# Performance work log

Hardware: AMD Instinct MI355X
Metric: run time of the kernel (lower is better)

The kernel has to match this reference:

```python
import jax, jax.numpy as jnp
import numpy as np

N_NODES = 500_000
N_ELEM = 2_000_000
W_AXIAL = 1.0
W_BENDING = 1.0


def _local_axes(x_local):
    # ref = [0,1,0] unless nearly parallel to x, then [0,0,1]
    parallel = jnp.abs(x_local[:, 1]) > 0.99
    ref = jnp.where(parallel[:, None],
                    jnp.array([0.0, 0.0, 1.0], x_local.dtype),
                    jnp.array([0.0, 1.0, 0.0], x_local.dtype))
    z = jnp.cross(x_local, ref)
    z = z / jnp.maximum(jnp.linalg.norm(z, axis=-1, keepdims=True), 1e-8)
    y = jnp.cross(z, x_local)
    y = y / jnp.maximum(jnp.linalg.norm(y, axis=-1, keepdims=True), 1e-8)
    return y, z


def setup_inputs() -> dict:
    key = jax.random.key(0)
    ks = jax.random.split(key, 10)
    pred = jax.random.normal(ks[0], (N_NODES, 6), jnp.float32) * 0.01
    connectivity = jax.random.randint(ks[1], (N_ELEM, 2), 0, N_NODES, dtype=jnp.int32)
    d = jax.random.normal(ks[2], (N_ELEM, 3), jnp.float32)
    elem_directions = d / jnp.linalg.norm(d, axis=-1, keepdims=True)
    elem_lengths = jax.random.uniform(ks[3], (N_ELEM,), jnp.float32, 0.5, 5.0)
    prop_E = jax.random.uniform(ks[4], (N_ELEM,), jnp.float32, 1e5, 2e6)
    prop_A = jax.random.uniform(ks[5], (N_ELEM,), jnp.float32, 0.01, 0.1)
    prop_I22 = jax.random.uniform(ks[6], (N_ELEM,), jnp.float32, 1e-5, 1e-3)
    line_load = jax.random.normal(ks[7], (N_NODES, 3), jnp.float32)
    bc_disp = jax.random.uniform(ks[8], (N_NODES, 1), jnp.float32)
    bc_rot = jax.random.uniform(ks[9], (N_NODES, 1), jnp.float32)
    return dict(pred=pred, connectivity=connectivity, elem_directions=elem_directions,
                elem_lengths=elem_lengths, prop_E=prop_E, prop_A=prop_A,
                prop_I22=prop_I22, line_load=line_load, bc_disp=bc_disp, bc_rot=bc_rot)


def reference(pred, connectivity, elem_directions, elem_lengths,
              prop_E, prop_A, prop_I22, line_load, bc_disp, bc_rot):
    n_nodes = pred.shape[0]
    u = pred[:, :3]
    theta = pred[:, 3:6]
    i_nodes = connectivity[:, 0]
    j_nodes = connectivity[:, 1]
    x_local = elem_directions
    y_local, z_local = _local_axes(x_local)
    L = elem_lengths

    du = u[j_nodes] - u[i_nodes]            # (E,3)
    th_i = theta[i_nodes]
    th_j = theta[j_nodes]

    # axial
    axial_disp = jnp.sum(du * x_local, axis=-1)
    N_axial = prop_E * prop_A / L * axial_disp
    F_axial_vec = N_axial[:, None] * x_local

    EI = prop_E * prop_I22
    L2 = L * L
    L3 = L2 * L

    # bending: transverse z (rotations about y)
    dw_z = jnp.sum(du * z_local, axis=-1)
    theta_yi = jnp.sum(th_i * y_local, axis=-1)
    theta_yj = jnp.sum(th_j * y_local, axis=-1)
    V_z = 12.0 * EI / L3 * dw_z + 6.0 * EI / L2 * (theta_yi + theta_yj)
    F_shear_vec = V_z[:, None] * z_local
    M_yi = 6.0 * EI / L2 * dw_z + EI / L * (2.0 * theta_yi + theta_yj)
    M_yj = 6.0 * EI / L2 * dw_z + EI / L * (theta_yi + 2.0 * theta_yj)
    M_vec_i = M_yi[:, None] * y_local
    M_vec_j = M_yj[:, None] * y_local

    # bending: transverse y (rotations about z)
    dw_y = jnp.sum(du * y_local, axis=-1)
    theta_zi = jnp.sum(th_i * z_local, axis=-1)
    theta_zj = jnp.sum(th_j * z_local, axis=-1)
    V_y = 12.0 * EI / L3 * dw_y + 6.0 * EI / L2 * (theta_zi + theta_zj)
    F_shear_y_vec = V_y[:, None] * y_local
    M_zi = 6.0 * EI / L2 * dw_y + EI / L * (2.0 * theta_zi + theta_zj)
    M_zj = 6.0 * EI / L2 * dw_y + EI / L * (theta_zi + 2.0 * theta_zj)
    M_vec_zi = M_zi[:, None] * z_local
    M_vec_zj = M_zj[:, None] * z_local

    # scatter to nodes (combined contributions, same sum as six scatter_adds)
    F_contrib = F_axial_vec + F_shear_vec + F_shear_y_vec
    F_total = jnp.zeros((n_nodes, 3), pred.dtype)
    F_total = F_total.at[i_nodes].add(F_contrib).at[j_nodes].add(-F_contrib)
    F_residual = F_total + line_load

    M_total = jnp.zeros((n_nodes, 3), pred.dtype)
    M_total = M_total.at[i_nodes].add(M_vec_i + M_vec_zi).at[j_nodes].add(M_vec_j + M_vec_zj)

    # characteristic scales
    F_char = jnp.maximum(jnp.mean(prop_E * prop_A), 1.0)
    M_char = jnp.maximum(jnp.mean(prop_E * prop_I22 / L), 1.0)

    # masked means over free nodes (== boolean-indexed .mean() in torch)
    free_disp = (bc_disp[:, 0] < 0.5).astype(pred.dtype)   # (N,)
    free_rot = (bc_rot[:, 0] < 0.5).astype(pred.dtype)
    sq_f = (F_residual / F_char) ** 2
    sq_m = (M_total / M_char) ** 2
    loss_force = jnp.sum(sq_f * free_disp[:, None]) / jnp.maximum(jnp.sum(free_disp) * 3.0, 1.0)
    loss_moment = jnp.sum(sq_m * free_rot[:, None]) / jnp.maximum(jnp.sum(free_rot) * 3.0, 1.0)
    return W_AXIAL * loss_force + W_BENDING * loss_moment
```

## Files before the change

### kernel.cpp

```cpp
#include <hip/hip_runtime.h>
#include <hip/hip_bf16.h>

#define N_NODES 500000
#define N_ELEM  2000000

#define CSH   11
#define NPBIN (1 << CSH)
#define NBIN  ((N_NODES + NPBIN - 1) >> CSH)
#define SBLK  256
#define CBLK  512

#define P16_OFF 32768ull
#define ENT_OFF (P16_OFF + 16ull * N_NODES)
#define WS_NEED (ENT_OFF + 16ull * 2 * N_ELEM)

__device__ __forceinline__ float wave_reduce(float v) {
    #pragma unroll
    for (int o = 32; o > 0; o >>= 1) v += __shfl_down(v, o, 64);
    return v;
}

template<int NW>
__device__ __forceinline__ void block_reduce_add(float v, double* dst, float* sm) {
    int lane = threadIdx.x & 63;
    int wave = threadIdx.x >> 6;
    v = wave_reduce(v);
    if (lane == 0) sm[wave] = v;
    __syncthreads();
    if (threadIdx.x == 0) {
        float s = 0.f;
        #pragma unroll
        for (int w = 0; w < NW; ++w) s += sm[w];
        atomicAdd(dst, (double)s);
    }
    __syncthreads();
}

__device__ __forceinline__ unsigned int pack2(float a, float b) {
    unsigned int ua = (__float_as_uint(a) + 0x8000u) >> 16;
    unsigned int ub = (__float_as_uint(b) + 0x8000u) & 0xFFFF0000u;
    return ua | ub;
}
__device__ __forceinline__ float unlo(unsigned int u) {
    return __uint_as_float(u << 16);
}
__device__ __forceinline__ float unhi(unsigned int u) {
    return __uint_as_float(u & 0xFFFF0000u);
}

__device__ __forceinline__ void beam_core(
    float x0, float x1, float x2,
    float u0i, float u1i, float u2i, float t0i, float t1i, float t2i,
    float u0j, float u1j, float u2j, float t0j, float t1j, float t2j,
    float L, float E, float A, float I,
    float& F0, float& F1, float& F2,
    float& Mi0, float& Mi1, float& Mi2,
    float& Mj0, float& Mj1, float& Mj2)
{
    bool par = fabsf(x1) > 0.99f;
    float r1 = par ? 0.f : 1.f;
    float r2 = par ? 1.f : 0.f;
    float z0 = x1 * r2 - x2 * r1;
    float z1 = -x0 * r2;
    float z2 = x0 * r1;
    float zn = fmaxf(sqrtf(z0 * z0 + z1 * z1 + z2 * z2), 1e-8f);
    float izn = 1.f / zn;
    z0 *= izn; z1 *= izn; z2 *= izn;
    float y0 = z1 * x2 - z2 * x1;
    float y1 = z2 * x0 - z0 * x2;
    float y2 = z0 * x1 - z1 * x0;
    float yn = fmaxf(sqrtf(y0 * y0 + y1 * y1 + y2 * y2), 1e-8f);
    float iyn = 1.f / yn;
    y0 *= iyn; y1 *= iyn; y2 *= iyn;

    float du0 = u0j - u0i;
    float du1 = u1j - u1i;
    float du2 = u2j - u2i;

    float EA = E * A;
    float EI = E * I;
    float invL = 1.f / L;
    float invL2 = invL * invL;
    float invL3 = invL2 * invL;

    float axial = du0 * x0 + du1 * x1 + du2 * x2;
    float Naxial = EA * invL * axial;

    float k12 = 12.f * EI * invL3;
    float k6  = 6.f * EI * invL2;
    float kL  = EI * invL;

    float dwz = du0 * z0 + du1 * z1 + du2 * z2;
    float tyi = t0i * y0 + t1i * y1 + t2i * y2;
    float tyj = t0j * y0 + t1j * y1 + t2j * y2;
    float Vz  = k12 * dwz + k6 * (tyi + tyj);
    float Myi = k6 * dwz + kL * (2.f * tyi + tyj);
    float Myj = k6 * dwz + kL * (tyi + 2.f * tyj);

    float dwy = du0 * y0 + du1 * y1 + du2 * y2;
    float tzi = t0i * z0 + t1i * z1 + t2i * z2;
    float tzj = t0j * z0 + t1j * z1 + t2j * z2;
    float Vy  = k12 * dwy + k6 * (tzi + tzj);
    float Mzi = k6 * dwy + kL * (2.f * tzi + tzj);
    float Mzj = k6 * dwy + kL * (tzi + 2.f * tzj);

    F0 = Naxial * x0 + Vz * z0 + Vy * y0;
    F1 = Naxial * x1 + Vz * z1 + Vy * y1;
    F2 = Naxial * x2 + Vz * z2 + Vy * y2;

    Mi0 = Myi * y0 + Mzi * z0;
    Mi1 = Myi * y1 + Mzi * z1;
    Mi2 = Myi * y2 + Mzi * z2;
    Mj0 = Myj * y0 + Mzj * z0;
    Mj1 = Myj * y1 + Mzj * z1;
    Mj2 = Myj * y2 + Mzj * z2;
}

__device__ __forceinline__ void beam_full(
    float x0, float x1, float x2,
    const float* __restrict__ pi, const float* __restrict__ pj,
    float L, float E, float A, float I,
    float& F0, float& F1, float& F2,
    float& Mi0, float& Mi1, float& Mi2,
    float& Mj0, float& Mj1, float& Mj2)
{
    float2 a0 = *(const float2*)(pi + 0);
    float2 a1 = *(const float2*)(pi + 2);
    float2 a2 = *(const float2*)(pi + 4);
    float2 b0 = *(const float2*)(pj + 0);
    float2 b1 = *(const float2*)(pj + 2);
    float2 b2 = *(const float2*)(pj + 4);
    beam_core(x0, x1, x2,
              a0.x, a0.y, a1.x, a1.y, a2.x, a2.y,
              b0.x, b0.y, b1.x, b1.y, b2.x, b2.y,
              L, E, A, I,
              F0, F1, F2, Mi0, Mi1, Mi2, Mj0, Mj1, Mj2);
}


__global__ __launch_bounds__(256) void prep_kernel(
    const float* __restrict__ pred, uint4* __restrict__ pred16)
{
    int n = blockIdx.x * 256 + threadIdx.x;
    if (n >= N_NODES) return;
    const float2* p2 = (const float2*)(pred + 6l * n);
    float2 a0 = p2[0], a1 = p2[1], a2 = p2[2];
    uint4 r;
    r.x = pack2(a0.x, a0.y);
    r.y = pack2(a1.x, a1.y);
    r.z = pack2(a2.x, a2.y);
    r.w = 0u;
    pred16[n] = r;
}


__global__ __launch_bounds__(256) void count_kernel(
    const int* __restrict__ conn, int* __restrict__ cnt)
{
    __shared__ int bins[NBIN];
    for (int i = threadIdx.x; i < NBIN; i += 256) bins[i] = 0;
    __syncthreads();

    int per = (N_ELEM + CBLK - 1) / CBLK;
    int e0 = blockIdx.x * per;
    int e1 = min(e0 + per, N_ELEM);
    const int2* c2 = (const int2*)conn;

    for (int e = e0 + threadIdx.x; e < e1; e += 256) {
        int2 c = c2[e];
        atomicAdd(&bins[c.x >> CSH], 1);
        atomicAdd(&bins[c.y >> CSH], 1);
    }
    __syncthreads();
    for (int i = threadIdx.x; i < NBIN; i += 256) {
        int c = bins[i];
        if (c) atomicAdd(&cnt[i], c);
    }
}

__global__ __launch_bounds__(256) void scan_kernel(
    const int* __restrict__ cnt,
    int* __restrict__ cur, int* __restrict__ off)
{
    __shared__ int s[256];
    int tid = threadIdx.x;
    int v = (tid < NBIN) ? cnt[tid] : 0;
    s[tid] = v;
    __syncthreads();
    for (int o = 1; o < 256; o <<= 1) {
        int t = (tid >= o) ? s[tid - o] : 0;
        __syncthreads();
        s[tid] += t;
        __syncthreads();
    }
    int excl = s[tid] - v;
    if (tid < NBIN) { off[tid] = excl; cur[tid] = excl; }
    if (tid == 255) off[NBIN] = s[255];
}


__global__ __launch_bounds__(1024) void emit_kernel(
    const uint4* __restrict__ pred16,
    const int* __restrict__ conn,
    const float* __restrict__ dirs,
    const float* __restrict__ L_, const float* __restrict__ E_,
    const float* __restrict__ A_, const float* __restrict__ I_,
    int* __restrict__ cur, uint4* __restrict__ ents,
    double* __restrict__ accum)
{
    __shared__ int bins[NBIN];
    __shared__ float sm[16];
    for (int i = threadIdx.x; i < NBIN; i += 1024) bins[i] = 0;
    __syncthreads();

    int per = (N_ELEM + SBLK - 1) / SBLK;
    int e0 = blockIdx.x * per;
    int e1 = min(e0 + per, N_ELEM);
    const int2* c2 = (const int2*)conn;

    for (int e = e0 + threadIdx.x; e < e1; e += 1024) {
        int2 c = c2[e];
        atomicAdd(&bins[c.x >> CSH], 1);
        atomicAdd(&bins[c.y >> CSH], 1);
    }
    __syncthreads();
    for (int i = threadIdx.x; i < NBIN; i += 1024) {
        int c = bins[i];
        bins[i] = c ? atomicAdd(&cur[i], c) : 0;
    }
    __syncthreads();

    float ea = 0.f, eil = 0.f;
    for (int e = e0 + threadIdx.x; e < e1; e += 1024) {
        int2 c = c2[e];
        uint4 pi = pred16[c.x];
        uint4 pj = pred16[c.y];
        float x0 = dirs[3 * e + 0], x1 = dirs[3 * e + 1], x2 = dirs[3 * e + 2];
        float L = L_[e], E = E_[e], A = A_[e], I = I_[e];
        ea  += E * A;
        eil += E * I / L;
        float F0, F1, F2, Mi0, Mi1, Mi2, Mj0, Mj1, Mj2;
        beam_core(x0, x1, x2,
                  unlo(pi.x), unhi(pi.x), unlo(pi.y), unhi(pi.y), unlo(pi.z), unhi(pi.z),
                  unlo(pj.x), unhi(pj.x), unlo(pj.y), unhi(pj.y), unlo(pj.z), unhi(pj.z),
                  L, E, A, I,
                  F0, F1, F2, Mi0, Mi1, Mi2, Mj0, Mj1, Mj2);

        int pi_ = atomicAdd(&bins[c.x >> CSH], 1);
        uint4 ei;
        ei.x = pack2(F0, F1);
        ei.y = pack2(F2, Mi0);
        ei.z = pack2(Mi1, Mi2);
        ei.w = (unsigned int)(c.x & (NPBIN - 1));
        ents[pi_] = ei;

        int pj_ = atomicAdd(&bins[c.y >> CSH], 1);
        uint4 ej;
        ej.x = pack2(-F0, -F1);
        ej.y = pack2(-F2, Mj0);
        ej.z = pack2(Mj1, Mj2);
        ej.w = (unsigned int)(c.y & (NPBIN - 1));
        ents[pj_] = ej;
    }
    block_reduce_add<16>(ea,  &accum[0], sm);
    block_reduce_add<16>(eil, &accum[1], sm);
}


__global__ __launch_bounds__(1024) void binacc_kernel(
    const uint4* __restrict__ ents,
    const int* __restrict__ off,
    const float* __restrict__ line_load,
    const float* __restrict__ bc_disp,
    const float* __restrict__ bc_rot,
    double* __restrict__ accum)
{
    __shared__ unsigned int acc3[NPBIN * 3];
    __shared__ float sm[16];
    int b = blockIdx.x;
    for (int i = threadIdx.x; i < NPBIN * 3; i += 1024) acc3[i] = 0u;
    __syncthreads();

    int s0 = off[b], s1 = off[b + 1];
    int nbase = b << CSH;
    unsigned int lds_base = (unsigned int)(unsigned long long)(&acc3[0]);

    int k = s0 + threadIdx.x;
    for (; k + 1024 < s1; k += 2048) {
        uint4 ea_ = ents[k];
        uint4 eb_ = ents[k + 1024];
        unsigned int aa = lds_base + ea_.w * 12u;
        unsigned int ab = lds_base + eb_.w * 12u;
        asm volatile(
            "ds_pk_add_bf16 %0, %2\n\t"
            "ds_pk_add_bf16 %0, %3 offset:4\n\t"
            "ds_pk_add_bf16 %0, %4 offset:8\n\t"
            "ds_pk_add_bf16 %1, %5\n\t"
            "ds_pk_add_bf16 %1, %6 offset:4\n\t"
            "ds_pk_add_bf16 %1, %7 offset:8"
            :: "v"(aa), "v"(ab),
               "v"(ea_.x), "v"(ea_.y), "v"(ea_.z),
               "v"(eb_.x), "v"(eb_.y), "v"(eb_.z)
            : "memory");
    }
    if (k < s1) {
        uint4 e = ents[k];
        unsigned int a = lds_base + e.w * 12u;
        asm volatile(
            "ds_pk_add_bf16 %0, %1\n\t"
            "ds_pk_add_bf16 %0, %2 offset:4\n\t"
            "ds_pk_add_bf16 %0, %3 offset:8"
            :: "v"(a), "v"(e.x), "v"(e.y), "v"(e.z)
            : "memory");
    }
    asm volatile("s_waitcnt lgkmcnt(0)" ::: "memory");
    __syncthreads();

    float sqF = 0.f, sqM = 0.f, fd = 0.f, fr = 0.f;
    for (int nl = threadIdx.x; nl < NPBIN; nl += 1024) {
        int n = nbase + nl;
        if (n < N_NODES) {
            float fdv = (bc_disp[n] < 0.5f) ? 1.f : 0.f;
            float frv = (bc_rot[n]  < 0.5f) ? 1.f : 0.f;
            unsigned int w0 = acc3[nl * 3 + 0];
            unsigned int w1 = acc3[nl * 3 + 1];
            unsigned int w2 = acc3[nl * 3 + 2];
            float Fr0 = unlo(w0) + line_load[3l * n + 0];
            float Fr1 = unhi(w0) + line_load[3l * n + 1];
            float Fr2 = unlo(w1) + line_load[3l * n + 2];
            float M0 = unhi(w1);
            float M1 = unlo(w2);
            float M2 = unhi(w2);
            sqF += fdv * (Fr0 * Fr0 + Fr1 * Fr1 + Fr2 * Fr2);
            sqM += frv * (M0 * M0 + M1 * M1 + M2 * M2);
            fd += fdv;
            fr += frv;
        }
    }
    block_reduce_add<16>(sqF, &accum[2], sm);
    block_reduce_add<16>(sqM, &accum[3], sm);
    block_reduce_add<16>(fd,  &accum[4], sm);
    block_reduce_add<16>(fr,  &accum[5], sm);
}

__global__ void final_kernel(const double* __restrict__ accum,
                             float* __restrict__ out)
{
    double F_char = fmax(accum[0] / (double)N_ELEM, 1.0);
    double M_char = fmax(accum[1] / (double)N_ELEM, 1.0);
    double lf = accum[2] / (F_char * F_char) / fmax(accum[4] * 3.0, 1.0);
    double lm = accum[3] / (M_char * M_char) / fmax(accum[5] * 3.0, 1.0);
    out[0] = (float)(lf + lm);
}


__global__ __launch_bounds__(256) void elem_kernel_fb(
    const float* __restrict__ pred,
    const int*   __restrict__ conn,
    const float* __restrict__ dirs,
    const float* __restrict__ L_, const float* __restrict__ E_,
    const float* __restrict__ A_, const float* __restrict__ I_,
    float* __restrict__ F_total, float* __restrict__ M_total,
    double* __restrict__ accum)
{
    __shared__ float sm[4];
    int e = blockIdx.x * blockDim.x + threadIdx.x;
    float ea = 0.f, eil = 0.f;
    if (e < N_ELEM) {
        int ni = conn[2 * e], nj = conn[2 * e + 1];
        float x0 = dirs[3 * e + 0], x1 = dirs[3 * e + 1], x2 = dirs[3 * e + 2];
        float L = L_[e], E = E_[e], A = A_[e], I = I_[e];
        float F0, F1, F2, Mi0, Mi1, Mi2, Mj0, Mj1, Mj2;
        beam_full(x0, x1, x2, pred + 6l * ni, pred + 6l * nj, L, E, A, I,
                  F0, F1, F2, Mi0, Mi1, Mi2, Mj0, Mj1, Mj2);
        atomicAdd(&F_total[3l * ni + 0],  F0);
        atomicAdd(&F_total[3l * ni + 1],  F1);
        atomicAdd(&F_total[3l * ni + 2],  F2);
        atomicAdd(&F_total[3l * nj + 0], -F0);
        atomicAdd(&F_total[3l * nj + 1], -F1);
        atomicAdd(&F_total[3l * nj + 2], -F2);
        atomicAdd(&M_total[3l * ni + 0], Mi0);
        atomicAdd(&M_total[3l * ni + 1], Mi1);
        atomicAdd(&M_total[3l * ni + 2], Mi2);
        atomicAdd(&M_total[3l * nj + 0], Mj0);
        atomicAdd(&M_total[3l * nj + 1], Mj1);
        atomicAdd(&M_total[3l * nj + 2], Mj2);
        ea  = E * A;
        eil = E * I / L;
    }
    block_reduce_add<4>(ea,  &accum[0], sm);
    block_reduce_add<4>(eil, &accum[1], sm);
}

__global__ __launch_bounds__(256) void node_kernel_fb(
    const float* __restrict__ F_total, const float* __restrict__ M_total,
    const float* __restrict__ line_load,
    const float* __restrict__ bc_disp, const float* __restrict__ bc_rot,
    double* __restrict__ accum)
{
    __shared__ float sm[4];
    int n = blockIdx.x * blockDim.x + threadIdx.x;
    float sqF = 0.f, sqM = 0.f, fd = 0.f, fr = 0.f;
    if (n < N_NODES) {
        fd = (bc_disp[n] < 0.5f) ? 1.f : 0.f;
        fr = (bc_rot[n]  < 0.5f) ? 1.f : 0.f;
        float Fr0 = F_total[3l * n + 0] + line_load[3l * n + 0];
        float Fr1 = F_total[3l * n + 1] + line_load[3l * n + 1];
        float Fr2 = F_total[3l * n + 2] + line_load[3l * n + 2];
        float M0 = M_total[3l * n + 0];
        float M1 = M_total[3l * n + 1];
        float M2 = M_total[3l * n + 2];
        sqF = fd * (Fr0 * Fr0 + Fr1 * Fr1 + Fr2 * Fr2);
        sqM = fr * (M0 * M0 + M1 * M1 + M2 * M2);
    }
    block_reduce_add<4>(sqF, &accum[2], sm);
    block_reduce_add<4>(sqM, &accum[3], sm);
    block_reduce_add<4>(fd,  &accum[4], sm);
    block_reduce_add<4>(fr,  &accum[5], sm);
}

extern "C" void kernel_launch(void* const* d_in, const int* in_sizes, int n_in,
                              void* d_out, int out_size, void* d_ws, size_t ws_size,
                              hipStream_t stream) {
    const float* pred      = (const float*)d_in[0];
    const int*   conn      = (const int*)  d_in[1];
    const float* dirs      = (const float*)d_in[2];
    const float* lens      = (const float*)d_in[3];
    const float* prop_E    = (const float*)d_in[4];
    const float* prop_A    = (const float*)d_in[5];
    const float* prop_I    = (const float*)d_in[6];
    const float* line_load = (const float*)d_in[7];
    const float* bc_disp   = (const float*)d_in[8];
    const float* bc_rot    = (const float*)d_in[9];

    double* accum = (double*)d_ws;

    if (ws_size >= WS_NEED) {
        int* off = (int*)((char*)d_ws + 1024);
        int* cnt = (int*)((char*)d_ws + 8192);
        int* cur = (int*)((char*)d_ws + 16384);
        uint4* pred16 = (uint4*)((char*)d_ws + P16_OFF);
        uint4* ents = (uint4*)((char*)d_ws + ENT_OFF);

        hipMemsetAsync(d_ws, 0, 32768, stream);

        prep_kernel<<<(N_NODES + 255) / 256, 256, 0, stream>>>(pred, pred16);
        count_kernel<<<CBLK, 256, 0, stream>>>(conn, cnt);
        scan_kernel<<<1, 256, 0, stream>>>(cnt, cur, off);
        emit_kernel<<<SBLK, 1024, 0, stream>>>(pred16, conn, dirs, lens,
                                               prop_E, prop_A, prop_I,
                                               cur, ents, accum);
        binacc_kernel<<<NBIN, 1024, 0, stream>>>(ents, off, line_load, bc_disp,
                                                 bc_rot, accum);
    } else {
        float* F_total = (float*)((char*)d_ws + 64);
        float* M_total = F_total + (size_t)N_NODES * 3;
        hipMemsetAsync(d_ws, 0, 64 + 2ull * N_NODES * 3 * sizeof(float), stream);
        int be = (N_ELEM + 255) / 256;
        elem_kernel_fb<<<be, 256, 0, stream>>>(pred, conn, dirs, lens, prop_E,
                                               prop_A, prop_I, F_total, M_total, accum);
        int bn = (N_NODES + 255) / 256;
        node_kernel_fb<<<bn, 256, 0, stream>>>(F_total, M_total, line_load,
                                               bc_disp, bc_rot, accum);
    }
    final_kernel<<<1, 1, 0, stream>>>(accum, (float*)d_out);
}
```

Measured before the change: 203.7 us.

## Precompute per-block bin offsets via histogram scan, remove emit-kernel recount

Count kernel now writes a per-block, per-bin histogram (ushort) that a new scan2 kernel prefix-sums across blocks, giving each emit block its exact base offsets. Emit no longer re-reads connectivity to count or does global atomics on bin cursors, and the bin width is halved (more, smaller bins) to give binacc more parallelism and a smaller working set per block. The cost is an extra kernel launch, extra histogram traffic, and a larger scan, and offsets are deterministic now.

```diff
diff --git a/kernel.cpp b/kernel.cpp
--- a/kernel.cpp
+++ b/kernel.cpp
@@ -4,15 +4,16 @@
 #define N_NODES 500000
 #define N_ELEM  2000000
 
-#define CSH   11
+#define CSH   10
 #define NPBIN (1 << CSH)
 #define NBIN  ((N_NODES + NPBIN - 1) >> CSH)
 #define SBLK  256
-#define CBLK  512
-
-#define P16_OFF 32768ull
-#define ENT_OFF (P16_OFF + 16ull * N_NODES)
-#define WS_NEED (ENT_OFF + 16ull * 2 * N_ELEM)
+
+#define HIST_OFF 16384ull
+#define OFFS_OFF 266752ull
+#define P16_OFF  524288ull
+#define ENT_OFF  (P16_OFF + 16ull * N_NODES)
+#define WS_NEED  (ENT_OFF + 16ull * 2 * N_ELEM)
 
 __device__ __forceinline__ float wave_reduce(float v) {
     #pragma unroll
@@ -155,14 +156,15 @@
 
 
 __global__ __launch_bounds__(256) void count_kernel(
-    const int* __restrict__ conn, int* __restrict__ cnt)
+    const int* __restrict__ conn, unsigned short* __restrict__ hist)
 {
     __shared__ int bins[NBIN];
     for (int i = threadIdx.x; i < NBIN; i += 256) bins[i] = 0;
     __syncthreads();
 
-    int per = (N_ELEM + CBLK - 1) / CBLK;
-    int e0 = blockIdx.x * per;
+    int b = blockIdx.x;
+    int per = (N_ELEM + SBLK - 1) / SBLK;
+    int e0 = b * per;
     int e1 = min(e0 + per, N_ELEM);
     const int2* c2 = (const int2*)conn;
 
@@ -172,30 +174,45 @@
         atomicAdd(&bins[c.y >> CSH], 1);
     }
     __syncthreads();
-    for (int i = threadIdx.x; i < NBIN; i += 256) {
-        int c = bins[i];
-        if (c) atomicAdd(&cnt[i], c);
-    }
-}
-
-__global__ __launch_bounds__(256) void scan_kernel(
-    const int* __restrict__ cnt,
-    int* __restrict__ cur, int* __restrict__ off)
+    for (int k = threadIdx.x; k < NBIN; k += 256)
+        hist[(size_t)k * SBLK + b] = (unsigned short)bins[k];
+}
+
+__global__ __launch_bounds__(256) void scan2_kernel(
+    const unsigned short* __restrict__ hist,
+    unsigned short* __restrict__ offs, int* __restrict__ cnt)
 {
     __shared__ int s[256];
+    int k = blockIdx.x, t = threadIdx.x;
+    int v = hist[(size_t)k * SBLK + t];
+    s[t] = v;
+    __syncthreads();
+    for (int o = 1; o < 256; o <<= 1) {
+        int tv = (t >= o) ? s[t - o] : 0;
+        __syncthreads();
+        s[t] += tv;
+        __syncthreads();
+    }
+    offs[(size_t)t * NBIN + k] = (unsigned short)(s[t] - v);
+    if (t == 255) cnt[k] = s[t];
+}
+
+__global__ __launch_bounds__(512) void scan_kernel(
+    const int* __restrict__ cnt, int* __restrict__ off)
+{
+    __shared__ int s[512];
     int tid = threadIdx.x;
     int v = (tid < NBIN) ? cnt[tid] : 0;
     s[tid] = v;
     __syncthreads();
-    for (int o = 1; o < 256; o <<= 1) {
+    for (int o = 1; o < 512; o <<= 1) {
         int t = (tid >= o) ? s[tid - o] : 0;
         __syncthreads();
         s[tid] += t;
         __syncthreads();
     }
-    int excl = s[tid] - v;
-    if (tid < NBIN) { off[tid] = excl; cur[tid] = excl; }
-    if (tid == 255) off[NBIN] = s[255];
+    if (tid < NBIN) off[tid] = s[tid] - v;
+    if (tid == 511) off[NBIN] = s[511];
 }
 
 
@@ -205,30 +222,20 @@
     const float* __restrict__ dirs,
     const float* __restrict__ L_, const float* __restrict__ E_,
     const float* __restrict__ A_, const float* __restrict__ I_,
-    int* __restrict__ cur, uint4* __restrict__ ents,
-    double* __restrict__ accum)
+    const int* __restrict__ off, const unsigned short* __restrict__ offs,
+    uint4* __restrict__ ents, double* __restrict__ accum)
 {
     __shared__ int bins[NBIN];
     __shared__ float sm[16];
-    for (int i = threadIdx.x; i < NBIN; i += 1024) bins[i] = 0;
+    int b = blockIdx.x;
+    for (int i = threadIdx.x; i < NBIN; i += 1024)
+        bins[i] = off[i] + (int)offs[(size_t)b * NBIN + i];
     __syncthreads();
 
     int per = (N_ELEM + SBLK - 1) / SBLK;
-    int e0 = blockIdx.x * per;
+    int e0 = b * per;
     int e1 = min(e0 + per, N_ELEM);
     const int2* c2 = (const int2*)conn;
-
-    for (int e = e0 + threadIdx.x; e < e1; e += 1024) {
-        int2 c = c2[e];
-        atomicAdd(&bins[c.x >> CSH], 1);
-        atomicAdd(&bins[c.y >> CSH], 1);
-    }
-    __syncthreads();
-    for (int i = threadIdx.x; i < NBIN; i += 1024) {
-        int c = bins[i];
-        bins[i] = c ? atomicAdd(&cur[i], c) : 0;
-    }
-    __syncthreads();
 
     float ea = 0.f, eil = 0.f;
     for (int e = e0 + threadIdx.x; e < e1; e += 1024) {
@@ -438,18 +445,20 @@
     if (ws_size >= WS_NEED) {
         int* off = (int*)((char*)d_ws + 1024);
         int* cnt = (int*)((char*)d_ws + 8192);
-        int* cur = (int*)((char*)d_ws + 16384);
+        unsigned short* hist = (unsigned short*)((char*)d_ws + HIST_OFF);
+        unsigned short* offs = (unsigned short*)((char*)d_ws + OFFS_OFF);
         uint4* pred16 = (uint4*)((char*)d_ws + P16_OFF);
         uint4* ents = (uint4*)((char*)d_ws + ENT_OFF);
 
-        hipMemsetAsync(d_ws, 0, 32768, stream);
+        hipMemsetAsync(d_ws, 0, 16384, stream);
 
         prep_kernel<<<(N_NODES + 255) / 256, 256, 0, stream>>>(pred, pred16);
-        count_kernel<<<CBLK, 256, 0, stream>>>(conn, cnt);
-        scan_kernel<<<1, 256, 0, stream>>>(cnt, cur, off);
+        count_kernel<<<SBLK, 256, 0, stream>>>(conn, hist);
+        scan2_kernel<<<NBIN, 256, 0, stream>>>(hist, offs, cnt);
+        scan_kernel<<<1, 512, 0, stream>>>(cnt, off);
         emit_kernel<<<SBLK, 1024, 0, stream>>>(pred16, conn, dirs, lens,
                                                prop_E, prop_A, prop_I,
-                                               cur, ents, accum);
+                                               off, offs, ents, accum);
         binacc_kernel<<<NBIN, 1024, 0, stream>>>(ents, off, line_load, bc_disp,
                                                  bc_rot, accum);
     } else {
```

Result: no change. 204.7 us (+0.5%).
